# Kernel tuning notes

Measured on AMD Instinct MI355X. Metric: run time of the kernel, lower is better.

## Reference

```python
import jax, jax.numpy as jnp
import numpy as np

N = 1_000_000          # number of query points
POINT_DIMS = 2         # (x, y) coordinates
NUM_EMB = 6572         # number of video frames
EMB_DIM = 32
HIDDEN = 128


def setup_inputs() -> dict:
    key = jax.random.key(0)
    ks = jax.random.split(key, 10)
    x = jax.random.uniform(ks[0], (N, POINT_DIMS), dtype=jnp.float32)
    # fractional frame index in [0, NUM_EMB - 1)
    embeddings = jax.random.uniform(ks[1], (N,), dtype=jnp.float32) * (NUM_EMB - 1)
    em_table = jax.random.normal(ks[2], (NUM_EMB, EMB_DIM), dtype=jnp.float32) * 0.1
    in0 = POINT_DIMS + EMB_DIM
    W0 = jax.random.normal(ks[3], (in0, HIDDEN), dtype=jnp.float32) / np.sqrt(in0)
    b0 = jax.random.normal(ks[4], (HIDDEN,), dtype=jnp.float32) * 0.01
    W1 = jax.random.normal(ks[5], (HIDDEN, HIDDEN), dtype=jnp.float32) / np.sqrt(HIDDEN)
    b1 = jax.random.normal(ks[6], (HIDDEN,), dtype=jnp.float32) * 0.01
    W2 = jax.random.normal(ks[7], (HIDDEN, 1), dtype=jnp.float32) / np.sqrt(HIDDEN)
    b2 = jax.random.normal(ks[8], (1,), dtype=jnp.float32) * 0.01
    return {"x": x, "embeddings": embeddings, "em_table": em_table,
            "W0": W0, "b0": b0, "W1": W1, "b1": b1, "W2": W2, "b2": b2}


def reference(x, embeddings, em_table, W0, b0, W1, b1, W2, b2):
    num_emb = em_table.shape[0]
    em1 = embeddings.astype(jnp.int32)                       # floor (inputs >= 0)
    em2 = jnp.minimum(em1 + 1, num_emb - 1)                  # clamp(em1+1, max=E-1)
    res = (embeddings - em1.astype(jnp.float32))[:, None]    # [N, 1]
    e1 = em_table[em1]                                       # [N, 32] gather
    e2 = em_table[em2]                                       # [N, 32] gather
    em = e1 + (e2 - e1) * res                                # lerp
    h = jnp.concatenate((x, em), axis=1) @ W0 + b0           # [N, 128]
    h = jnp.clip(h, 0.0, 1.0)
    h = jnp.clip(h @ W1 + b1, 0.0, 1.0)
    out = jax.nn.sigmoid(h @ W2 + b2)                        # [N, 1]
    return out
```

## Files before the change

### kernel.cpp

```cpp
#include <hip/hip_runtime.h>
#include <hip/hip_bf16.h>


using bf16x8 = __attribute__((ext_vector_type(8))) short;
using f32x4  = __attribute__((ext_vector_type(4))) float;

#define NPTS    1000000
#define NUMEMB  6572
#define HID     128
#define M_IT    64
#define A0S     72
#define H0S     136
#define TILES   (NPTS / M_IT)
#define NBLOCKS 768

__device__ __forceinline__ unsigned short bf16r(float f) {
    unsigned u;
    __builtin_memcpy(&u, &f, 4);
    u = (u + 0x7fffu + ((u >> 16) & 1u)) >> 16;
    return (unsigned short)u;
}
__device__ __forceinline__ unsigned pk2(float a, float b) {
    float2 f2; f2.x = a; f2.y = b;
    __hip_bfloat162 h = __float22bfloat162_rn(f2);
    unsigned u;
    __builtin_memcpy(&u, &h, 4);
    return u;
}
__device__ __forceinline__ unsigned pk2c(float a, float b) {
    unsigned r;
    asm("v_cvt_pk_bf16_f32 %0, %1, %2 clamp" : "=v"(r) : "v"(a), "v"(b));
    return r;
}
__device__ __forceinline__ void bar_lds() {
    asm volatile("s_waitcnt lgkmcnt(0)\n\ts_barrier" ::: "memory");
}

__global__ __launch_bounds__(256, 3)
void mlp_fused(const float* __restrict__ x,
               const float* __restrict__ emb,
               const float* __restrict__ em_table,
               const float* __restrict__ W0, const float* __restrict__ b0,
               const float* __restrict__ W1, const float* __restrict__ b1,
               const float* __restrict__ W2, const float* __restrict__ b2,
               float* __restrict__ out)
{
    __shared__ __align__(16) unsigned short A0[M_IT * A0S];
    __shared__ __align__(16) unsigned short H0[M_IT * H0S];

    const int tid  = threadIdx.x;
    const int lane = tid & 63;
    const int nq   = tid >> 6;
    const int q    = lane >> 4;
    const int cl   = lane & 15;
    const int p    = tid >> 2;
    const int s    = tid & 3;

    for (int i = tid; i < M_IT * A0S; i += 256) A0[i] = 0;

    const int hcol = nq * 32 + (cl >> 2) * 8 + (cl & 3);
    bf16x8 w0t[2][2];
    for (int hb = 0; hb < 2; ++hb)
        for (int kt = 0; kt < 2; ++kt) {
            const int col = hcol + hb * 4;
            bf16x8 v;
            #pragma unroll
            for (int e = 0; e < 8; ++e) {
                const int k = kt * 32 + q * 8 + e;
                float val = 0.f;
                if (k < 32)       val = W0[(2 + k) * HID + col];
                else if (k == 32) val = W0[0 * HID + col];
                else if (k == 33) val = W0[1 * HID + col];
                v[e] = (short)bf16r(val);
            }
            w0t[hb][kt] = v;
        }

    bf16x8 w1r[2][4];
    for (int hb = 0; hb < 2; ++hb)
        for (int kk = 0; kk < 4; ++kk) {
            const int kt  = (nq + kk) & 3;
            const int col = hcol + hb * 4;
            bf16x8 v;
            #pragma unroll
            for (int e = 0; e < 8; ++e) {
                const int k = kt * 32 + q * 8 + e;
                v[e] = (short)bf16r(W1[k * HID + col]);
            }
            w1r[hb][kk] = v;
        }

    f32x4 b0q[2], b1q[2];
    for (int hb = 0; hb < 2; ++hb)
        for (int r = 0; r < 4; ++r) {
            const int h = nq * 32 + q * 8 + hb * 4 + r;
            b0q[hb][r] = b0[h];
            b1q[hb][r] = b1[h];
        }
    bf16x8 w2f;
    #pragma unroll
    for (int e = 0; e < 8; ++e)
        w2f[e] = (cl == 0) ? (short)bf16r(W2[nq * 32 + q * 8 + e]) : (short)0;
    const float bias2 = b2[0];

    int t = blockIdx.x;
    float  feA;
    float2 xvA = {0.f, 0.f};
    {
        const int gp = t * M_IT + p;
        feA = emb[gp];
        if (s == 0) xvA = *(const float2*)(x + 2 * gp);
    }

    __syncthreads();

    int prev_base = -1;

    for (; t < TILES; t += gridDim.x) {
        const int base = t * M_IT;

        {
            const int e1 = (int)feA;
            const int e2 = (e1 + 1 < NUMEMB) ? e1 + 1 : NUMEMB - 1;
            const float r = feA - (float)e1;
            const float4* p1 = (const float4*)(em_table + e1 * 32 + s * 8);
            const float4* p2 = (const float4*)(em_table + e2 * 32 + s * 8);
            const float4 a0v = p1[0], a1v = p1[1];
            const float4 c0v = p2[0], c1v = p2[1];
            uint4 d;
            d.x = pk2(a0v.x + (c0v.x - a0v.x) * r, a0v.y + (c0v.y - a0v.y) * r);
            d.y = pk2(a0v.z + (c0v.z - a0v.z) * r, a0v.w + (c0v.w - a0v.w) * r);
            d.z = pk2(a1v.x + (c1v.x - a1v.x) * r, a1v.y + (c1v.y - a1v.y) * r);
            d.w = pk2(a1v.z + (c1v.z - a1v.z) * r, a1v.w + (c1v.w - a1v.w) * r);
            *(uint4*)&A0[p * A0S + s * 8] = d;
            if (s == 0) *(unsigned*)&A0[p * A0S + 32] = pk2(xvA.x, xvA.y);
        }
        bar_lds();

        if (prev_base >= 0 && tid < 64) {
            const float4 pv = *(const float4*)((const char*)A0 + tid * 144 + 128);
            const float zz = bias2 + pv.x + pv.y + pv.z + pv.w;
            out[prev_base + tid] = __builtin_amdgcn_rcpf(1.f + __expf(-zz));
        }

        f32x4 acc[4][2];
        #pragma unroll
        for (int pb = 0; pb < 4; ++pb) {
            const bf16x8 bf0 = *(const bf16x8*)&A0[(pb * 16 + cl) * A0S + q * 8];
            const bf16x8 bf1 = *(const bf16x8*)&A0[(pb * 16 + cl) * A0S + 32 + q * 8];
            #pragma unroll
            for (int hb = 0; hb < 2; ++hb) {
                f32x4 a = __builtin_amdgcn_mfma_f32_16x16x32_bf16(
                    w0t[hb][0], bf0, b0q[hb], 0, 0, 0);
                acc[pb][hb] = __builtin_amdgcn_mfma_f32_16x16x32_bf16(
                    w0t[hb][1], bf1, a, 0, 0, 0);
            }
        }

        {
            int t1 = t + gridDim.x; if (t1 >= TILES) t1 = t;
            const int gp = t1 * M_IT + p;
            feA = emb[gp];
            if (s == 0) xvA = *(const float2*)(x + 2 * gp);
        }

        #pragma unroll
        for (int pb = 0; pb < 4; ++pb) {
            const f32x4 v0 = acc[pb][0], v1 = acc[pb][1];
            uint4 w;
            w.x = pk2c(v0[0], v0[1]);
            w.y = pk2c(v0[2], v0[3]);
            w.z = pk2c(v1[0], v1[1]);
            w.w = pk2c(v1[2], v1[3]);
            *(uint4*)&H0[(pb * 16 + cl) * H0S + nq * 32 + q * 8] = w;
        }
        bar_lds();

        #pragma unroll
        for (int kk = 0; kk < 4; ++kk) {
            const int kcol = (((nq + kk) & 3) << 5) + q * 8;
            #pragma unroll
            for (int pb = 0; pb < 4; ++pb) {
                bf16x8 bfrag = *(const bf16x8*)
                    &H0[(pb * 16 + cl) * H0S + kcol];
                #pragma unroll
                for (int hb = 0; hb < 2; ++hb)
                    acc[pb][hb] = __builtin_amdgcn_mfma_f32_16x16x32_bf16(
                        w1r[hb][kk], bfrag,
                        kk == 0 ? b1q[hb] : acc[pb][hb], 0, 0, 0);
            }
        }

        const f32x4 zero = {0.f, 0.f, 0.f, 0.f};
        #pragma unroll
        for (int pb = 0; pb < 4; ++pb) {
            const f32x4 v0 = acc[pb][0], v1 = acc[pb][1];
            uint4 w;
            w.x = pk2c(v0[0], v0[1]);
            w.y = pk2c(v0[2], v0[3]);
            w.z = pk2c(v1[0], v1[1]);
            w.w = pk2c(v1[2], v1[3]);
            bf16x8 hf;
            __builtin_memcpy(&hf, &w, 16);
            const f32x4 z4 = __builtin_amdgcn_mfma_f32_16x16x32_bf16(
                w2f, hf, zero, 0, 0, 0);
            if (q == 0)
                *(float*)((char*)A0 + (pb * 16 + cl) * 144 + 128 + nq * 4) = z4[0];
        }
        prev_base = base;

    }

    bar_lds();
    if (prev_base >= 0 && tid < 64) {
        const float4 pv = *(const float4*)((const char*)A0 + tid * 144 + 128);
        const float zz = bias2 + pv.x + pv.y + pv.z + pv.w;
        out[prev_base + tid] = __builtin_amdgcn_rcpf(1.f + __expf(-zz));
    }
}

extern "C" void kernel_launch(void* const* d_in, const int* in_sizes, int n_in,
                              void* d_out, int out_size, void* d_ws, size_t ws_size,
                              hipStream_t stream) {
    const float* x   = (const float*)d_in[0];
    const float* emb = (const float*)d_in[1];
    const float* emt = (const float*)d_in[2];
    const float* W0  = (const float*)d_in[3];
    const float* b0  = (const float*)d_in[4];
    const float* W1  = (const float*)d_in[5];
    const float* b1  = (const float*)d_in[6];
    const float* W2  = (const float*)d_in[7];
    const float* b2  = (const float*)d_in[8];
    mlp_fused<<<NBLOCKS, 256, 0, stream>>>(x, emb, emt, W0, b0, W1, b1, W2, b2,
                                           (float*)d_out);
}
```

Before: 120.8 us.

## Double-buffer the embedding-gather tile and prefetch the gather one tile ahead

The A0 input tile becomes two LDS buffers. The em_table gather for the next tile is issued before the layer-0 MFMAs and its lerp result is written into the alternate buffer afterwards. Embedding indices and x coordinates are now prefetched two tiles ahead, and a prologue fills the first buffer before the loop. The aim is to hide global gather latency behind matrix work, at the cost of extra LDS and more live registers under the 3-blocks-per-CU launch bound.

```diff
diff --git a/kernel.cpp b/kernel.cpp
--- a/kernel.cpp
+++ b/kernel.cpp
@@ -45,7 +45,7 @@
                const float* __restrict__ W2, const float* __restrict__ b2,
                float* __restrict__ out)
 {
-    __shared__ __align__(16) unsigned short A0[M_IT * A0S];
+    __shared__ __align__(16) unsigned short A0[2 * M_IT * A0S];
     __shared__ __align__(16) unsigned short H0[M_IT * H0S];
 
     const int tid  = threadIdx.x;
@@ -56,7 +56,7 @@
     const int p    = tid >> 2;
     const int s    = tid & 3;
 
-    for (int i = tid; i < M_IT * A0S; i += 256) A0[i] = 0;
+    for (int i = tid; i < 2 * M_IT * A0S; i += 256) A0[i] = 0;
 
     const int hcol = nq * 32 + (cl >> 2) * 8 + (cl & 3);
     bf16x8 w0t[2][2];
@@ -111,30 +111,34 @@
         feA = emb[gp];
         if (s == 0) xvA = *(const float2*)(x + 2 * gp);
     }
-
     __syncthreads();
+    {
+        const int e1 = (int)feA;
+        const int e2 = (e1 + 1 < NUMEMB) ? e1 + 1 : NUMEMB - 1;
+        const float r = feA - (float)e1;
+        const float4* p1 = (const float4*)(em_table + e1 * 32 + s * 8);
+        const float4* p2 = (const float4*)(em_table + e2 * 32 + s * 8);
+        const float4 a0v = p1[0], a1v = p1[1];
+        const float4 c0v = p2[0], c1v = p2[1];
+        uint4 d;
+        d.x = pk2(a0v.x + (c0v.x - a0v.x) * r, a0v.y + (c0v.y - a0v.y) * r);
+        d.y = pk2(a0v.z + (c0v.z - a0v.z) * r, a0v.w + (c0v.w - a0v.w) * r);
+        d.z = pk2(a1v.x + (c1v.x - a1v.x) * r, a1v.y + (c1v.y - a1v.y) * r);
+        d.w = pk2(a1v.z + (c1v.z - a1v.z) * r, a1v.w + (c1v.w - a1v.w) * r);
+        *(uint4*)&A0[p * A0S + s * 8] = d;
+        if (s == 0) *(unsigned*)&A0[p * A0S + 32] = pk2(xvA.x, xvA.y);
+    }
+    {
+        int t1 = t + NBLOCKS; if (t1 >= TILES) t1 = t;
+        const int gp = t1 * M_IT + p;
+        feA = emb[gp];
+        if (s == 0) xvA = *(const float2*)(x + 2 * gp);
+    }
 
     int prev_base = -1;
-
-    for (; t < TILES; t += gridDim.x) {
+    int buf = 0;
+    for (; t < TILES; t += NBLOCKS) {
         const int base = t * M_IT;
-
-        {
-            const int e1 = (int)feA;
-            const int e2 = (e1 + 1 < NUMEMB) ? e1 + 1 : NUMEMB - 1;
-            const float r = feA - (float)e1;
-            const float4* p1 = (const float4*)(em_table + e1 * 32 + s * 8);
-            const float4* p2 = (const float4*)(em_table + e2 * 32 + s * 8);
-            const float4 a0v = p1[0], a1v = p1[1];
-            const float4 c0v = p2[0], c1v = p2[1];
-            uint4 d;
-            d.x = pk2(a0v.x + (c0v.x - a0v.x) * r, a0v.y + (c0v.y - a0v.y) * r);
-            d.y = pk2(a0v.z + (c0v.z - a0v.z) * r, a0v.w + (c0v.w - a0v.w) * r);
-            d.z = pk2(a1v.x + (c1v.x - a1v.x) * r, a1v.y + (c1v.y - a1v.y) * r);
-            d.w = pk2(a1v.z + (c1v.z - a1v.z) * r, a1v.w + (c1v.w - a1v.w) * r);
-            *(uint4*)&A0[p * A0S + s * 8] = d;
-            if (s == 0) *(unsigned*)&A0[p * A0S + 32] = pk2(xvA.x, xvA.y);
-        }
         bar_lds();
 
         if (prev_base >= 0 && tid < 64) {
@@ -143,11 +147,30 @@
             out[prev_base + tid] = __builtin_amdgcn_rcpf(1.f + __expf(-zz));
         }
 
+        const int ge1 = (int)feA;
+        const int ge2 = (ge1 + 1 < NUMEMB) ? ge1 + 1 : NUMEMB - 1;
+        const float frA = feA - (float)ge1;
+        const float4* pg1 = (const float4*)(em_table + ge1 * 32 + s * 8);
+        const float4* pg2 = (const float4*)(em_table + ge2 * 32 + s * 8);
+        const float4 g1a = pg1[0], g1b = pg1[1];
+        const float4 g2a = pg2[0], g2b = pg2[1];
+        float feN;
+        float2 xvN = {0.f, 0.f};
+        {
+            int t2 = t + 2 * NBLOCKS; if (t2 >= TILES) t2 = t;
+            const int gp = t2 * M_IT + p;
+            feN = emb[gp];
+            if (s == 0) xvN = *(const float2*)(x + 2 * gp);
+        }
+
+        const int aB = buf * (M_IT * A0S);
         f32x4 acc[4][2];
         #pragma unroll
         for (int pb = 0; pb < 4; ++pb) {
-            const bf16x8 bf0 = *(const bf16x8*)&A0[(pb * 16 + cl) * A0S + q * 8];
-            const bf16x8 bf1 = *(const bf16x8*)&A0[(pb * 16 + cl) * A0S + 32 + q * 8];
+            const bf16x8 bf0 = *(const bf16x8*)
+                &A0[aB + (pb * 16 + cl) * A0S + q * 8];
+            const bf16x8 bf1 = *(const bf16x8*)
+                &A0[aB + (pb * 16 + cl) * A0S + 32 + q * 8];
             #pragma unroll
             for (int hb = 0; hb < 2; ++hb) {
                 f32x4 a = __builtin_amdgcn_mfma_f32_16x16x32_bf16(
@@ -158,11 +181,16 @@
         }
 
         {
-            int t1 = t + gridDim.x; if (t1 >= TILES) t1 = t;
-            const int gp = t1 * M_IT + p;
-            feA = emb[gp];
-            if (s == 0) xvA = *(const float2*)(x + 2 * gp);
-        }
+            const int sB = (buf ^ 1) * (M_IT * A0S);
+            uint4 d;
+            d.x = pk2(g1a.x + (g2a.x - g1a.x) * frA, g1a.y + (g2a.y - g1a.y) * frA);
+            d.y = pk2(g1a.z + (g2a.z - g1a.z) * frA, g1a.w + (g2a.w - g1a.w) * frA);
+            d.z = pk2(g1b.x + (g2b.x - g1b.x) * frA, g1b.y + (g2b.y - g1b.y) * frA);
+            d.w = pk2(g1b.z + (g2b.z - g1b.z) * frA, g1b.w + (g2b.w - g1b.w) * frA);
+            *(uint4*)&A0[sB + p * A0S + s * 8] = d;
+            if (s == 0) *(unsigned*)&A0[sB + p * A0S + 32] = pk2(xvA.x, xvA.y);
+        }
+        feA = feN; xvA = xvN;
 
         #pragma unroll
         for (int pb = 0; pb < 4; ++pb) {
@@ -208,7 +236,7 @@
                 *(float*)((char*)A0 + (pb * 16 + cl) * 144 + 128 + nq * 4) = z4[0];
         }
         prev_base = base;
-
+        buf ^= 1;
     }
 
     bar_lds();
```

Result: slower. 124.3 us (+2.9%).
